# Performance work log

Measured on AMD Instinct MI355X. Metric: run time of the kernel, lower is better.

## Reference

```python
import jax, jax.numpy as jnp
import numpy as np

B, T, CM, CZ, H = 2, 512, 256, 128, 16
DH = CM // H  # 16
EPS = 1e-5


def setup_inputs() -> dict:
    root = jax.random.key(0)
    ks = jax.random.split(root, 16)
    n = lambda i, shape: jax.random.normal(ks[i], shape, dtype=jnp.float32)
    s = np.float32(1.0 / np.sqrt(CM))
    return dict(
        query=n(0, (B, T, CM)),
        key=n(1, (B, T, CM)),
        value=n(2, (B, T, CM)),
        pos_embedding=n(3, (B, 2 * T - 1, CM)),  # T2 = 2T-1 relative positions
        z=n(4, (B, T, T, CZ)),
        mask=jax.random.randint(ks[5], (B, 1, T), 0, 2) > 0,
        Wq=n(6, (CM, CM)) * s, bq=jnp.zeros((CM,), jnp.float32),
        Wk=n(7, (CM, CM)) * s, bk=jnp.zeros((CM,), jnp.float32),
        Wv=n(8, (CM, CM)) * s, bv=jnp.zeros((CM,), jnp.float32),
        Wp=n(9, (CM, CM)) * s,
        u_bias=n(10, (H, DH)) * np.float32(0.1),
        v_bias=n(11, (H, DH)) * np.float32(0.1),
        Wo=n(12, (CM, CM)) * s, bo=jnp.zeros((CM,), jnp.float32),
        ln_g=jnp.ones((CZ,), jnp.float32), ln_b=jnp.zeros((CZ,), jnp.float32),
        Wz=n(13, (CZ, H)) * np.float32(1.0 / np.sqrt(CZ)),
    )


def _relative_shift(ps):
    # ps: (B, H, T1, T2) -> Transformer-XL relative shift, keep first T2//2+1 cols
    b, h, t1, t2 = ps.shape
    padded = jnp.pad(ps, ((0, 0), (0, 0), (0, 0), (1, 0)))  # (b,h,t1,t2+1)
    padded = padded.reshape(b, h, t2 + 1, t1)
    shifted = padded[:, :, 1:, :].reshape(b, h, t1, t2)
    return shifted[..., : t2 // 2 + 1]


def reference(query, key, value, pos_embedding, z, mask,
              Wq, bq, Wk, bk, Wv, bv, Wp, u_bias, v_bias, Wo, bo,
              ln_g, ln_b, Wz):
    b = query.shape[0]
    q = (query @ Wq.T + bq).reshape(b, -1, H, DH)          # (b,T,H,dh)
    k = (key @ Wk.T + bk).reshape(b, -1, H, DH)
    v = (value @ Wv.T + bv).reshape(b, -1, H, DH)
    p = (pos_embedding @ Wp.T).reshape(b, -1, H, DH)       # (b,2T-1,H,dh)

    content = jnp.einsum('bihd,bjhd->bhij', q + u_bias, k)     # (b,H,T,T)
    pos = jnp.einsum('bihd,bjhd->bhij', q + v_bias, p)         # (b,H,T,2T-1)
    pos = _relative_shift(pos)                                  # (b,H,T,T)

    # z bias: LayerNorm over c_z then project to heads (chunking in torch is a no-op math-wise)
    mu = jnp.mean(z, axis=-1, keepdims=True)
    var = jnp.var(z, axis=-1, keepdims=True)
    zn = (z - mu) * jax.lax.rsqrt(var + EPS) * ln_g + ln_b
    z_bias = jnp.einsum('bijc,ch->bhij', zn, Wz)                # (b,H,T,T)

    score = (content + pos) / np.float32(np.sqrt(DH)) + z_bias
    score = jnp.where(mask[:, None, :, :], jnp.float32(-10000.0), score)
    attn = jax.nn.softmax(score, axis=-1)  # dropout is identity in eval

    ctx = jnp.einsum('bhij,bjhd->bihd', attn, v).reshape(b, -1, CM)
    return ctx @ Wo.T + bo
```

## Files before the change

kernel.cpp:

```cpp
#include <hip/hip_runtime.h>
#include <hip/hip_bf16.h>

typedef __attribute__((ext_vector_type(8))) short short8;
typedef __attribute__((ext_vector_type(4))) short short4v;
typedef __attribute__((ext_vector_type(4))) float f32x4;

#define LD4(dst, v4) { dst[0]=(v4).x; dst[1]=(v4).y; dst[2]=(v4).z; dst[3]=(v4).w; }

static __device__ __forceinline__ short f2bf(float f) {
    union { float f; unsigned u; } v; v.f = f;
    unsigned r = (v.u + 0x7FFFu + ((v.u >> 16) & 1u)) >> 16;
    return (short)r;
}
static __device__ __forceinline__ float bf2f(short s) {
    union { unsigned u; float f; } v; v.u = ((unsigned)(unsigned short)s) << 16;
    return v.f;
}
static __device__ __forceinline__ unsigned cvt_pk_bf16(float lo, float hi) {
    unsigned r;
    asm volatile("v_cvt_pk_bf16_f32 %0, %1, %2" : "=v"(r) : "v"(lo), "v"(hi));
    return r;
}

static __device__ __forceinline__ void proj_tile(
    const float* __restrict__ X, const float* __restrict__ W,
    const float* __restrict__ bias, float* __restrict__ Yf,
    short* __restrict__ Yb, int M, int base, float* xs)
{
    int rt = base >> 1, ct = base & 1;
    int t = threadIdx.x;
    int row_base = rt * 32;
    {
        int r = t >> 3, k0 = (t & 7) * 32;
        int row = row_base + r;
        if (row < M) {
            const float* xp = X + (size_t)row * 256 + k0;
            #pragma unroll
            for (int q = 0; q < 8; ++q) {
                float4 v = *(const float4*)(xp + q * 4);
                xs[(k0 + q * 4 + 0) * 36 + r] = v.x;
                xs[(k0 + q * 4 + 1) * 36 + r] = v.y;
                xs[(k0 + q * 4 + 2) * 36 + r] = v.z;
                xs[(k0 + q * 4 + 3) * 36 + r] = v.w;
            }
        } else {
            #pragma unroll
            for (int q = 0; q < 32; ++q) xs[(k0 + q) * 36 + r] = 0.f;
        }
    }
    __syncthreads();
    int c_base = ct * 128 + (t & 31) * 4;
    int r_base = (t >> 5) * 4;
    float acc[4][4];
    #pragma unroll
    for (int a = 0; a < 4; ++a)
        #pragma unroll
        for (int b = 0; b < 4; ++b) acc[a][b] = 0.f;
    for (int k = 0; k < 256; k += 4) {
        float w0[4], w1[4], w2[4], w3[4];
        { float4 v = *(const float4*)(W + (size_t)(c_base + 0) * 256 + k); LD4(w0, v); }
        { float4 v = *(const float4*)(W + (size_t)(c_base + 1) * 256 + k); LD4(w1, v); }
        { float4 v = *(const float4*)(W + (size_t)(c_base + 2) * 256 + k); LD4(w2, v); }
        { float4 v = *(const float4*)(W + (size_t)(c_base + 3) * 256 + k); LD4(w3, v); }
        #pragma unroll
        for (int kk = 0; kk < 4; ++kk) {
            float xl[4];
            float4 xv = *(const float4*)(&xs[(k + kk) * 36 + r_base]);
            LD4(xl, xv);
            #pragma unroll
            for (int ri = 0; ri < 4; ++ri) {
                acc[ri][0] += xl[ri] * w0[kk];
                acc[ri][1] += xl[ri] * w1[kk];
                acc[ri][2] += xl[ri] * w2[kk];
                acc[ri][3] += xl[ri] * w3[kk];
            }
        }
    }
    #pragma unroll
    for (int ri = 0; ri < 4; ++ri) {
        int row = row_base + r_base + ri;
        if (row < M) {
            float o0 = acc[ri][0] + (bias ? bias[c_base + 0] : 0.f);
            float o1 = acc[ri][1] + (bias ? bias[c_base + 1] : 0.f);
            float o2 = acc[ri][2] + (bias ? bias[c_base + 2] : 0.f);
            float o3 = acc[ri][3] + (bias ? bias[c_base + 3] : 0.f);
            if (Yb) {
                short4v o; o[0] = f2bf(o0); o[1] = f2bf(o1); o[2] = f2bf(o2); o[3] = f2bf(o3);
                *(short4v*)(Yb + (size_t)row * 256 + c_base) = o;
            } else {
                float4 o; o.x = o0; o.y = o1; o.z = o2; o.w = o3;
                *(float4*)(Yf + (size_t)row * 256 + c_base) = o;
            }
        }
    }
}

__global__ void k_proj(const float* __restrict__ query, const float* __restrict__ key,
                       const float* __restrict__ value, const float* __restrict__ pos,
                       const float* __restrict__ Wq, const float* __restrict__ bq,
                       const float* __restrict__ Wk, const float* __restrict__ bk,
                       const float* __restrict__ Wv, const float* __restrict__ bv,
                       const float* __restrict__ Wp,
                       const float* __restrict__ ln_g, const float* __restrict__ ln_b,
                       const float* __restrict__ Wz, const int* __restrict__ mask,
                       float* __restrict__ qb, short* __restrict__ kbf,
                       short* __restrict__ vbf, short* __restrict__ pbf,
                       short* __restrict__ wzp, float* __restrict__ Ah, float* __restrict__ Ch,
                       int* __restrict__ idx, int* __restrict__ cnt)
{
    __shared__ float xs[256 * 36];
    int bx = blockIdx.x;
    if (bx == 320) {
        int lane = threadIdx.x & 63, wave = threadIdx.x >> 6;
        if (wave == 0) {
            for (int b = 0; b < 2; ++b) {
                int* idxb = idx + b * 512;
                #pragma unroll
                for (int q = 0; q < 8; ++q) idxb[q * 64 + lane] = -1;
                int total = 0;
                for (int q = 0; q < 8; ++q) {
                    int j = q * 64 + lane;
                    int u = (mask[b * 512 + j] == 0) ? 1 : 0;
                    unsigned long long bal = __ballot(u);
                    int p = total + __popcll(bal & ((1ull << lane) - 1ull));
                    if (u) idxb[p] = j;
                    total += (int)__popcll(bal);
                }
                if (total == 0) {
                    for (int q = 0; q < 8; ++q) idxb[q * 64 + lane] = q * 64 + lane;
                    total = 512;
                }
                if (lane == 0) cnt[b] = total;
            }
        } else if (wave == 1) {
            for (int id = lane; id < 2048; id += 64) {
                int m = id >> 9, rem = id & 511, l = rem >> 3, ii = rem & 7;
                int c = m * 32 + ((l >> 4) << 3) + ii, h = l & 15;
                wzp[id] = f2bf(ln_g[c] * Wz[c * 16 + h]);
            }
        } else if (wave == 2) {
            int h = lane & 15, part = lane >> 4;
            float a = 0.f, c = 0.f;
            #pragma unroll 4
            for (int cc = part * 32; cc < part * 32 + 32; ++cc) {
                float wv = Wz[cc * 16 + h];
                a += ln_g[cc] * wv;
                c += ln_b[cc] * wv;
            }
            a += __shfl_xor(a, 16); a += __shfl_xor(a, 32);
            c += __shfl_xor(c, 16); c += __shfl_xor(c, 32);
            if (part == 0) { Ah[h] = a; Ch[h] = c; }
        }
        return;
    }
    if (bx < 64)       proj_tile(query, Wq, bq, qb, nullptr, 1024, bx, xs);
    else if (bx < 128) proj_tile(key,   Wk, bk, nullptr, kbf, 1024, bx - 64, xs);
    else if (bx < 192) proj_tile(value, Wv, bv, nullptr, vbf, 1024, bx - 128, xs);
    else               proj_tile(pos,   Wp, nullptr, nullptr, pbf, 2046, bx - 192, xs);
}

__global__ void k_compact(const int* __restrict__ idx,
                          const short* __restrict__ kbf, const short* __restrict__ vbf,
                          short* __restrict__ kbfC, short* __restrict__ vbTC)
{
    __shared__ short st[32 * 264];
    const short8 z8v = {0,0,0,0,0,0,0,0};
    int bx = blockIdx.x;
    int b = bx >> 4, jn0 = (bx & 15) * 32;
    int t = threadIdx.x;
    int r = t >> 3, cc = (t & 7) * 32;
    int jn = jn0 + r;
    int jv = idx[b * 512 + jn];
    {
        short* dst = kbfC + ((size_t)b * 512 + jn) * 256 + cc;
        if (jv >= 0) {
            const short* src = kbf + ((size_t)b * 512 + jv) * 256 + cc;
            #pragma unroll
            for (int q = 0; q < 4; ++q) *(short8*)(dst + q * 8) = *(const short8*)(src + q * 8);
        } else {
            #pragma unroll
            for (int q = 0; q < 4; ++q) *(short8*)(dst + q * 8) = z8v;
        }
    }
    {
        if (jv >= 0) {
            const short* src = vbf + ((size_t)b * 512 + jv) * 256 + cc;
            #pragma unroll
            for (int q = 0; q < 4; ++q) *(short8*)(&st[r * 264 + cc + q * 8]) = *(const short8*)(src + q * 8);
        } else {
            #pragma unroll
            for (int q = 0; q < 4; ++q) *(short8*)(&st[r * 264 + cc + q * 8]) = z8v;
        }
        __syncthreads();
        int c = t;
        short tmp[32];
        #pragma unroll
        for (int q = 0; q < 32; ++q) tmp[q] = st[q * 264 + c];
        short* dst = vbTC + ((size_t)b * 256 + c) * 512 + jn0;
        #pragma unroll
        for (int q = 0; q < 4; ++q) *(short8*)(dst + q * 8) = *(const short8*)(&tmp[q * 8]);
    }
}

__global__ void __launch_bounds__(256, 2) k_attn_z(
    const float* __restrict__ z,
    const float* __restrict__ qb, const short* __restrict__ kbfC, const short* __restrict__ pbf,
    const short* __restrict__ wzp, const float* __restrict__ Ah, const float* __restrict__ Ch,
    const float* __restrict__ u_bias, const float* __restrict__ v_bias,
    const int* __restrict__ idx, const int* __restrict__ cnt,
    const short* __restrict__ vbTC,
    const float* __restrict__ Wo, const float* __restrict__ bo, float* __restrict__ out)
{
    __shared__ __align__(16) char lds_raw[53248];
    float* scf    = (float*)lds_raw;
    short* zs_all = (short*)(lds_raw + 34816);
    short* wT     = (short*)(lds_raw + 34816);
    float* redm   = (float*)(lds_raw + 51712);
    float* reds   = (float*)(lds_raw + 51968);
    float* ctxl   = (float*)(lds_raw + 52224);
    const short8 zero8 = {0, 0, 0, 0, 0, 0, 0, 0};

    int bi = blockIdx.x;
    int b = bi >> 9, i = bi & 511;
    int t = threadIdx.x;
    int lane = t & 63, wave = t >> 6;
    int h = lane & 15, g = lane >> 4;
    int l5 = lane >> 5, l31 = lane & 31;
    int np = (min(cnt[b], 512) + 31) & ~31;
    int nt16 = np >> 4;
    short* zs = zs_all + wave * 2112;
    const float* zb_ = z + (size_t)bi * 65536;

    short8 wz[4];
    #pragma unroll
    for (int m = 0; m < 4; ++m) wz[m] = *(const short8*)(wzp + m * 512 + lane * 8);
    float ah = Ah[h], ch = Ch[h];

    bool act = ((h & 1) == (g >> 1));
    int m_act = act ? (h >> 1) : 8;
    short8 qu8 = zero8, qv8 = zero8;
    {
        int c0q = h * 16 + (g & 1) * 8;
        const float* qp = qb + (size_t)bi * 256 + c0q;
        #pragma unroll
        for (int ii = 0; ii < 8; ++ii) {
            float qv_ = qp[ii];
            qu8[ii] = f2bf(0.25f * (qv_ + u_bias[c0q + ii]));
            qv8[ii] = f2bf(0.25f * (qv_ + v_bias[c0q + ii]));
        }
        if (!act) { qu8 = zero8; qv8 = zero8; }
    }

    int idxq[8];
    #pragma unroll
    for (int q = 0; q < 8; ++q) {
        int tl = wave + q * 4;
        idxq[q] = (tl < nt16) ? idx[b * 512 + tl * 16 + h] : -1;
    }

    float mloc = -3.0e38f;
    #pragma unroll
    for (int q = 0; q < 8; ++q) {
        int tl = wave + q * 4;
        if (tl < nt16) {
            float4 zv[8];
            #pragma unroll
            for (int m = 0; m < 8; ++m) {
                int r = 2 * m + l5;
                int jv = __shfl(idxq[q], r);
                int jr = (jv < 0) ? 0 : jv;
                zv[m] = *(const float4*)(zb_ + (size_t)jr * 128 + l31 * 4);
            }
            int jn = tl * 16 + h;
            int jvh = idxq[q];
            int jrp = 511 + ((jvh < 0) ? 0 : jvh) - i;
            const short* kr = kbfC + ((size_t)b * 512 + jn) * 256 + g * 8;
            const short* pr = pbf + ((size_t)b * 1023 + jrp) * 256 + g * 8;
            f32x4 acp = {0.f, 0.f, 0.f, 0.f};
            #pragma unroll
            for (int m = 0; m < 8; ++m) {
                short8 ka = *(const short8*)(kr + m * 32);
                short8 pa = *(const short8*)(pr + m * 32);
                short8 bu = (m == m_act) ? qu8 : zero8;
                short8 bv = (m == m_act) ? qv8 : zero8;
                acp = __builtin_amdgcn_mfma_f32_16x16x32_bf16(ka, bu, acp, 0, 0, 0);
                acp = __builtin_amdgcn_mfma_f32_16x16x32_bf16(pa, bv, acp, 0, 0, 0);
            }
            #pragma unroll
            for (int m = 0; m < 8; ++m) {
                int r = 2 * m + l5;
                uint2 pk;
                pk.x = cvt_pk_bf16(zv[m].x, zv[m].y);
                pk.y = cvt_pk_bf16(zv[m].z, zv[m].w);
                *(uint2*)(&zs[r * 132 + l31 * 4]) = pk;
            }
            short8 af[4];
            float sum = 0.f, sq = 0.f;
            #pragma unroll
            for (int m = 0; m < 4; ++m) {
                short4v a0 = *(const short4v*)(&zs[h * 132 + g * 8 + m * 32]);
                short4v a1 = *(const short4v*)(&zs[h * 132 + g * 8 + m * 32 + 4]);
                short8 s8;
                s8[0] = a0[0]; s8[1] = a0[1]; s8[2] = a0[2]; s8[3] = a0[3];
                s8[4] = a1[0]; s8[5] = a1[1]; s8[6] = a1[2]; s8[7] = a1[3];
                af[m] = s8;
                #pragma unroll
                for (int ii = 0; ii < 8; ++ii) {
                    float x = bf2f(s8[ii]);
                    sum += x;
                    sq = fmaf(x, x, sq);
                }
            }
            sum += __shfl_xor(sum, 16); sum += __shfl_xor(sum, 32);
            sq  += __shfl_xor(sq, 16);  sq  += __shfl_xor(sq, 32);
            float mu = sum * (1.f / 128.f);
            float rs = rsqrtf(sq * (1.f / 128.f) - mu * mu + 1e-5f);
            f32x4 accz = {0.f, 0.f, 0.f, 0.f};
            #pragma unroll
            for (int m = 0; m < 4; ++m)
                accz = __builtin_amdgcn_mfma_f32_16x16x32_bf16(af[m], wz[m], accz, 0, 0, 0);
            #pragma unroll
            for (int reg = 0; reg < 4; ++reg) {
                int orow = g * 4 + reg;
                float mo = __shfl(mu, orow);
                float ro = __shfl(rs, orow);
                int jj = __shfl(idxq[q], orow);
                float s = acp[reg] + ro * (accz[reg] - mo * ah) + ch;
                s = (jj < 0) ? -3.0e38f : s;
                scf[(tl * 16 + orow) * 17 + h] = s;
                mloc = fmaxf(mloc, s);
            }
        }
    }

    mloc = fmaxf(mloc, __shfl_xor(mloc, 16));
    mloc = fmaxf(mloc, __shfl_xor(mloc, 32));
    redm[wave * 16 + h] = mloc;
    __syncthreads();
    float mg = fmaxf(fmaxf(redm[h], redm[16 + h]), fmaxf(redm[32 + h], redm[48 + h]));
    float ssum = 0.f;
    for (int q = 0; q < 8; ++q) {
        int tl = wave + q * 4;
        if (tl < nt16) {
            #pragma unroll
            for (int reg = 0; reg < 4; ++reg) {
                int j = tl * 16 + g * 4 + reg;
                float e = __expf(scf[j * 17 + h] - mg);
                ssum += e;
                scf[j * 17 + h] = e;
            }
        }
    }
    ssum += __shfl_xor(ssum, 16); ssum += __shfl_xor(ssum, 32);
    reds[wave * 16 + h] = ssum;
    __syncthreads();
    float sg = reds[h] + reds[16 + h] + reds[32 + h] + reds[48 + h];
    float inv = 1.f / sg;
    for (int q = 0; q < 8; ++q) {
        int tl = wave + q * 4;
        if (tl < nt16) {
            short4v w4;
            #pragma unroll
            for (int reg = 0; reg < 4; ++reg)
                w4[reg] = f2bf(scf[(tl * 16 + g * 4 + reg) * 17 + h] * inv);
            *(short4v*)(&wT[h * 520 + tl * 16 + g * 4]) = w4;
        }
    }
    __syncthreads();

    #pragma unroll
    for (int q = 0; q < 4; ++q) {
        int hp = wave * 4 + q;
        int c0 = hp * 16;
        const short* vrow = vbTC + ((size_t)b * 256 + c0 + h) * 512;
        f32x4 a0 = {0.f, 0.f, 0.f, 0.f};
        for (int jn0 = 0; jn0 < np; jn0 += 32) {
            short8 wA = *(const short8*)(&wT[hp * 520 + jn0 + g * 8]);
            short8 vB = *(const short8*)(vrow + jn0 + g * 8);
            a0 = __builtin_amdgcn_mfma_f32_16x16x32_bf16(wA, vB, a0, 0, 0, 0);
        }
        if (g == 0) ctxl[c0 + h] = a0[0];
    }
    __syncthreads();

    {
        float acc = bo[t];
        const float* wrow = Wo + (size_t)t * 256;
        #pragma unroll 4
        for (int k = 0; k < 256; k += 8) {
            float4 w0 = *(const float4*)(wrow + k);
            float4 w1 = *(const float4*)(wrow + k + 4);
            acc += ctxl[k + 0] * w0.x + ctxl[k + 1] * w0.y
                 + ctxl[k + 2] * w0.z + ctxl[k + 3] * w0.w
                 + ctxl[k + 4] * w1.x + ctxl[k + 5] * w1.y
                 + ctxl[k + 6] * w1.z + ctxl[k + 7] * w1.w;
        }
        out[(size_t)bi * 256 + t] = acc;
    }
}

extern "C" void kernel_launch(void* const* d_in, const int* in_sizes, int n_in,
                              void* d_out, int out_size, void* d_ws, size_t ws_size,
                              hipStream_t stream) {
    const float* query = (const float*)d_in[0];
    const float* key   = (const float*)d_in[1];
    const float* value = (const float*)d_in[2];
    const float* pos   = (const float*)d_in[3];
    const float* z     = (const float*)d_in[4];
    const int*   mask  = (const int*)d_in[5];
    const float* Wq = (const float*)d_in[6];
    const float* bq = (const float*)d_in[7];
    const float* Wk = (const float*)d_in[8];
    const float* bk = (const float*)d_in[9];
    const float* Wv = (const float*)d_in[10];
    const float* bv = (const float*)d_in[11];
    const float* Wp = (const float*)d_in[12];
    const float* u_bias = (const float*)d_in[13];
    const float* v_bias = (const float*)d_in[14];
    const float* Wo = (const float*)d_in[15];
    const float* bo = (const float*)d_in[16];
    const float* ln_g = (const float*)d_in[17];
    const float* ln_b = (const float*)d_in[18];
    const float* Wz = (const float*)d_in[19];

    char* ws = (char*)d_ws;
    float* qb   = (float*)(ws + 0);
    short* kbf  = (short*)(ws + (1u << 20));
    short* vbf  = (short*)(ws + 1572864u);
    short* pbf  = (short*)(ws + (2u << 20));
    short* wzp  = (short*)(ws + (3u << 20));
    float* Ah   = (float*)(ws + (3u << 20) + 4096);
    float* Ch   = (float*)(ws + (3u << 20) + 4160);
    int*   idx  = (int*)(ws + (3u << 20) + 8192);
    int*   cnt  = (int*)(ws + (3u << 20) + 16384);
    short* kbfC = (short*)(ws + (4u << 20));
    short* vbTC = (short*)(ws + 4718592u);

    hipLaunchKernelGGL(k_proj, dim3(321), dim3(256), 0, stream,
                       query, key, value, pos, Wq, bq, Wk, bk, Wv, bv, Wp,
                       ln_g, ln_b, Wz, mask,
                       qb, kbf, vbf, pbf, wzp, Ah, Ch, idx, cnt);
    hipLaunchKernelGGL(k_compact, dim3(32), dim3(256), 0, stream,
                       idx, kbf, vbf, kbfC, vbTC);
    hipLaunchKernelGGL(k_attn_z, dim3(1024), dim3(256), 0, stream,
                       z, qb, kbfC, pbf, wzp, Ah, Ch, u_bias, v_bias, idx, cnt, vbTC,
                       Wo, bo, (float*)d_out);
}
```

Before: 154.8 us.

## Eliminate compaction kernel; gather K by index and write V transposed in projection

Removes the separate k_compact launch. The value projection now writes V directly in a transposed bf16 layout through an LDS staging tile, and the attention kernel reads K rows through the unmasked-index table instead of a compacted copy. The softmax weights are scattered into a zeroed full-length LDS row at their original key positions, so the PV MFMA loop now always covers all 512 keys rather than only the unmasked count. This saves one launch and a copy pass, but adds an LDS zero-fill and roughly doubles the PV MFMA work when about half the keys are masked. The transposed V store also writes scalar shorts.

```diff
diff --git a/kernel.cpp b/kernel.cpp
--- a/kernel.cpp
+++ b/kernel.cpp
@@ -25,7 +25,7 @@
 static __device__ __forceinline__ void proj_tile(
     const float* __restrict__ X, const float* __restrict__ W,
     const float* __restrict__ bias, float* __restrict__ Yf,
-    short* __restrict__ Yb, int M, int base, float* xs)
+    short* __restrict__ Yb, short* __restrict__ Yt, int M, int base, float* xs)
 {
     int rt = base >> 1, ct = base & 1;
     int t = threadIdx.x;
@@ -76,6 +76,27 @@
             }
         }
     }
+    if (Yt) {
+        short* xt = (short*)xs;
+        __syncthreads();
+        #pragma unroll
+        for (int ri = 0; ri < 4; ++ri) {
+            #pragma unroll
+            for (int cj = 0; cj < 4; ++cj) {
+                int c_local = (t & 31) * 4 + cj;
+                float bv_ = bias ? bias[ct * 128 + c_local] : 0.f;
+                xt[c_local * 34 + r_base + ri] = f2bf(acc[ri][cj] + bv_);
+            }
+        }
+        __syncthreads();
+        int c_local = t >> 1, half = t & 1;
+        int bb = row_base >> 9, j0 = (row_base & 511) + half * 16;
+        short* dst = Yt + ((size_t)bb * 256 + ct * 128 + c_local) * 512 + j0;
+        const short* src = xt + c_local * 34 + half * 16;
+        #pragma unroll
+        for (int qq = 0; qq < 16; ++qq) dst[qq] = src[qq];
+        return;
+    }
     #pragma unroll
     for (int ri = 0; ri < 4; ++ri) {
         int row = row_base + r_base + ri;
@@ -104,7 +125,7 @@
                        const float* __restrict__ ln_g, const float* __restrict__ ln_b,
                        const float* __restrict__ Wz, const int* __restrict__ mask,
                        float* __restrict__ qb, short* __restrict__ kbf,
-                       short* __restrict__ vbf, short* __restrict__ pbf,
+                       short* __restrict__ vbT, short* __restrict__ pbf,
                        short* __restrict__ wzp, float* __restrict__ Ah, float* __restrict__ Ch,
                        int* __restrict__ idx, int* __restrict__ cnt)
 {
@@ -153,62 +174,19 @@
         }
         return;
     }
-    if (bx < 64)       proj_tile(query, Wq, bq, qb, nullptr, 1024, bx, xs);
-    else if (bx < 128) proj_tile(key,   Wk, bk, nullptr, kbf, 1024, bx - 64, xs);
-    else if (bx < 192) proj_tile(value, Wv, bv, nullptr, vbf, 1024, bx - 128, xs);
-    else               proj_tile(pos,   Wp, nullptr, nullptr, pbf, 2046, bx - 192, xs);
-}
-
-__global__ void k_compact(const int* __restrict__ idx,
-                          const short* __restrict__ kbf, const short* __restrict__ vbf,
-                          short* __restrict__ kbfC, short* __restrict__ vbTC)
-{
-    __shared__ short st[32 * 264];
-    const short8 z8v = {0,0,0,0,0,0,0,0};
-    int bx = blockIdx.x;
-    int b = bx >> 4, jn0 = (bx & 15) * 32;
-    int t = threadIdx.x;
-    int r = t >> 3, cc = (t & 7) * 32;
-    int jn = jn0 + r;
-    int jv = idx[b * 512 + jn];
-    {
-        short* dst = kbfC + ((size_t)b * 512 + jn) * 256 + cc;
-        if (jv >= 0) {
-            const short* src = kbf + ((size_t)b * 512 + jv) * 256 + cc;
-            #pragma unroll
-            for (int q = 0; q < 4; ++q) *(short8*)(dst + q * 8) = *(const short8*)(src + q * 8);
-        } else {
-            #pragma unroll
-            for (int q = 0; q < 4; ++q) *(short8*)(dst + q * 8) = z8v;
-        }
-    }
-    {
-        if (jv >= 0) {
-            const short* src = vbf + ((size_t)b * 512 + jv) * 256 + cc;
-            #pragma unroll
-            for (int q = 0; q < 4; ++q) *(short8*)(&st[r * 264 + cc + q * 8]) = *(const short8*)(src + q * 8);
-        } else {
-            #pragma unroll
-            for (int q = 0; q < 4; ++q) *(short8*)(&st[r * 264 + cc + q * 8]) = z8v;
-        }
-        __syncthreads();
-        int c = t;
-        short tmp[32];
-        #pragma unroll
-        for (int q = 0; q < 32; ++q) tmp[q] = st[q * 264 + c];
-        short* dst = vbTC + ((size_t)b * 256 + c) * 512 + jn0;
-        #pragma unroll
-        for (int q = 0; q < 4; ++q) *(short8*)(dst + q * 8) = *(const short8*)(&tmp[q * 8]);
-    }
+    if (bx < 64)       proj_tile(query, Wq, bq, qb, nullptr, nullptr, 1024, bx, xs);
+    else if (bx < 128) proj_tile(key,   Wk, bk, nullptr, kbf, nullptr, 1024, bx - 64, xs);
+    else if (bx < 192) proj_tile(value, Wv, bv, nullptr, nullptr, vbT, 1024, bx - 128, xs);
+    else               proj_tile(pos,   Wp, nullptr, nullptr, pbf, nullptr, 2046, bx - 192, xs);
 }
 
 __global__ void __launch_bounds__(256, 2) k_attn_z(
     const float* __restrict__ z,
-    const float* __restrict__ qb, const short* __restrict__ kbfC, const short* __restrict__ pbf,
+    const float* __restrict__ qb, const short* __restrict__ kbf, const short* __restrict__ pbf,
     const short* __restrict__ wzp, const float* __restrict__ Ah, const float* __restrict__ Ch,
     const float* __restrict__ u_bias, const float* __restrict__ v_bias,
     const int* __restrict__ idx, const int* __restrict__ cnt,
-    const short* __restrict__ vbTC,
+    const short* __restrict__ vbT,
     const float* __restrict__ Wo, const float* __restrict__ bo, float* __restrict__ out)
 {
     __shared__ __align__(16) char lds_raw[53248];
@@ -271,10 +249,10 @@
                 int jr = (jv < 0) ? 0 : jv;
                 zv[m] = *(const float4*)(zb_ + (size_t)jr * 128 + l31 * 4);
             }
-            int jn = tl * 16 + h;
             int jvh = idxq[q];
-            int jrp = 511 + ((jvh < 0) ? 0 : jvh) - i;
-            const short* kr = kbfC + ((size_t)b * 512 + jn) * 256 + g * 8;
+            int jr = (jvh < 0) ? 0 : jvh;
+            int jrp = 511 + jr - i;
+            const short* kr = kbf + ((size_t)(b * 512 + jr)) * 256 + g * 8;
             const short* pr = pbf + ((size_t)b * 1023 + jrp) * 256 + g * 8;
             f32x4 acp = {0.f, 0.f, 0.f, 0.f};
             #pragma unroll
@@ -356,14 +334,24 @@
     __syncthreads();
     float sg = reds[h] + reds[16 + h] + reds[32 + h] + reds[48 + h];
     float inv = 1.f / sg;
+
+    {
+        int* wTi = (int*)wT;
+        for (int o = t; o < 4160; o += 256) wTi[o] = 0;
+    }
+    __syncthreads();
     for (int q = 0; q < 8; ++q) {
         int tl = wave + q * 4;
         if (tl < nt16) {
-            short4v w4;
-            #pragma unroll
-            for (int reg = 0; reg < 4; ++reg)
-                w4[reg] = f2bf(scf[(tl * 16 + g * 4 + reg) * 17 + h] * inv);
-            *(short4v*)(&wT[h * 520 + tl * 16 + g * 4]) = w4;
+            int4 jv4 = *(const int4*)(idx + b * 512 + tl * 16 + g * 4);
+            int jj4[4]; jj4[0] = jv4.x; jj4[1] = jv4.y; jj4[2] = jv4.z; jj4[3] = jv4.w;
+            #pragma unroll
+            for (int reg = 0; reg < 4; ++reg) {
+                if (jj4[reg] >= 0) {
+                    float w = scf[(tl * 16 + g * 4 + reg) * 17 + h] * inv;
+                    wT[h * 520 + jj4[reg]] = f2bf(w);
+                }
+            }
         }
     }
     __syncthreads();
@@ -372,9 +360,9 @@
     for (int q = 0; q < 4; ++q) {
         int hp = wave * 4 + q;
         int c0 = hp * 16;
-        const short* vrow = vbTC + ((size_t)b * 256 + c0 + h) * 512;
+        const short* vrow = vbT + ((size_t)b * 256 + c0 + h) * 512;
         f32x4 a0 = {0.f, 0.f, 0.f, 0.f};
-        for (int jn0 = 0; jn0 < np; jn0 += 32) {
+        for (int jn0 = 0; jn0 < 512; jn0 += 32) {
             short8 wA = *(const short8*)(&wT[hp * 520 + jn0 + g * 8]);
             short8 vB = *(const short8*)(vrow + jn0 + g * 8);
             a0 = __builtin_amdgcn_mfma_f32_16x16x32_bf16(wA, vB, a0, 0, 0, 0);
@@ -426,23 +414,19 @@
     char* ws = (char*)d_ws;
     float* qb   = (float*)(ws + 0);
     short* kbf  = (short*)(ws + (1u << 20));
-    short* vbf  = (short*)(ws + 1572864u);
+    short* vbT  = (short*)(ws + 1572864u);
     short* pbf  = (short*)(ws + (2u << 20));
     short* wzp  = (short*)(ws + (3u << 20));
     float* Ah   = (float*)(ws + (3u << 20) + 4096);
     float* Ch   = (float*)(ws + (3u << 20) + 4160);
     int*   idx  = (int*)(ws + (3u << 20) + 8192);
     int*   cnt  = (int*)(ws + (3u << 20) + 16384);
-    short* kbfC = (short*)(ws + (4u << 20));
-    short* vbTC = (short*)(ws + 4718592u);
 
     hipLaunchKernelGGL(k_proj, dim3(321), dim3(256), 0, stream,
                        query, key, value, pos, Wq, bq, Wk, bk, Wv, bv, Wp,
                        ln_g, ln_b, Wz, mask,
-                       qb, kbf, vbf, pbf, wzp, Ah, Ch, idx, cnt);
-    hipLaunchKernelGGL(k_compact, dim3(32), dim3(256), 0, stream,
-                       idx, kbf, vbf, kbfC, vbTC);
+                       qb, kbf, vbT, pbf, wzp, Ah, Ch, idx, cnt);
     hipLaunchKernelGGL(k_attn_z, dim3(1024), dim3(256), 0, stream,
-                       z, qb, kbfC, pbf, wzp, Ah, Ch, u_bias, v_bias, idx, cnt, vbTC,
+                       z, qb, kbf, pbf, wzp, Ah, Ch, u_bias, v_bias, idx, cnt, vbT,
                        Wo, bo, (float*)d_out);
 }
```

New measurement: 161.4 us. +4.3%, slower.
